# Optimization experiments

Measured on AMD Instinct MI355X. Metric: run time of the kernel, lower is better.

## Reference

```python
import jax, jax.numpy as jnp
import numpy as np
from jax.ops import segment_sum, segment_max

# Graph layout: B contiguous graphs of NPER nodes each
N, B, NPER, E, K = 32768, 32, 1024, 524288, 32
IN_DIM, HID = 64, 64
H1, H2 = 4, 2
NEG_ATTN, NEG_ACT = 0.2, 0.01  # DGL GATConv leaky slope; module's LeakyReLU slope


def _gat(x, src, dst, W, al, ar, H, D):
    # DGL GATConv, no bias, no residual, dropout=0
    f = (x @ W).reshape(N, H, D)                      # [N,H,D]
    el = jnp.einsum('nhd,hd->nh', f, al)              # src attention term
    er = jnp.einsum('nhd,hd->nh', f, ar)              # dst attention term
    e = jax.nn.leaky_relu(el[src] + er[dst], NEG_ATTN)  # [E,H]
    m = segment_max(e, dst, num_segments=N)
    m = jnp.where(jnp.isfinite(m), m, 0.0)            # guard isolated nodes
    p = jnp.exp(e - m[dst])
    z = segment_sum(p, dst, num_segments=N)
    a = p / jnp.maximum(z[dst], 1e-9)                 # edge softmax over in-edges
    return segment_sum(a[:, :, None] * f[src], dst, num_segments=N)  # [N,H,D]


def _graphnorm(x, alpha, gamma, beta, eps=1e-5):
    # GraphNorm (Cai et al.): per-graph node normalization with learnable mean scale
    xb = x.reshape(B, NPER, *x.shape[1:])
    mean = xb.mean(axis=1, keepdims=True)
    c = xb - alpha * mean
    var = (c * c).mean(axis=1, keepdims=True)
    return (gamma * c / jnp.sqrt(var + eps) + beta).reshape(x.shape)


def _sortpool(x):
    # DGL SortPooling: sort each node's features ascending, pick top-K nodes by last channel
    xs = jnp.sort(x, axis=-1).reshape(B, NPER, -1)
    _, idx = jax.lax.top_k(xs[:, :, -1], K)           # [B,K]
    sel = jnp.take_along_axis(xs, idx[:, :, None], axis=1)  # [B,K,D]
    return sel.reshape(B, -1)


def setup_inputs() -> dict:
    key = jax.random.key(0)
    ks = jax.random.split(key, 16)
    rng = np.random.default_rng(0)
    # edges constrained within each contiguous graph block
    g = rng.integers(0, B, size=E)
    src = (g * NPER + rng.integers(0, NPER, size=E)).astype(np.int32)
    dst = (g * NPER + rng.integers(0, NPER, size=E)).astype(np.int32)
    s = 0.05
    return {
        'features': jax.random.normal(ks[0], (N, IN_DIM), jnp.float32),
        'src': jnp.asarray(src), 'dst': jnp.asarray(dst),
        'W1': jax.random.normal(ks[1], (IN_DIM, H1 * HID), jnp.float32) * s,
        'al1': jax.random.normal(ks[2], (H1, HID), jnp.float32) * s,
        'ar1': jax.random.normal(ks[3], (H1, HID), jnp.float32) * s,
        'W2': jax.random.normal(ks[4], (H1 * HID, H2 * HID), jnp.float32) * s,
        'al2': jax.random.normal(ks[5], (H2, HID), jnp.float32) * s,
        'ar2': jax.random.normal(ks[6], (H2, HID), jnp.float32) * s,
        'gn1_alpha': jnp.ones((HID,), jnp.float32),
        'gn1_gamma': jnp.ones((HID,), jnp.float32),
        'gn1_beta': jnp.zeros((HID,), jnp.float32),
        'gn2_alpha': jnp.ones((HID,), jnp.float32),
        'gn2_gamma': jnp.ones((HID,), jnp.float32),
        'gn2_beta': jnp.zeros((HID,), jnp.float32),
        'fc1_w': jax.random.normal(ks[7], (2 * K * HID, K * HID), jnp.float32) * 0.02,
        'fc1_b': jnp.zeros((K * HID,), jnp.float32),
        'fc2_w': jax.random.normal(ks[8], (K * HID, 16), jnp.float32) * 0.02,
        'fc2_b': jnp.zeros((16,), jnp.float32),
    }


def reference(features, src, dst, W1, al1, ar1, W2, al2, ar2,
              gn1_alpha, gn1_gamma, gn1_beta, gn2_alpha, gn2_gamma, gn2_beta,
              fc1_w, fc1_b, fc2_w, fc2_b):
    h1 = _gat(features, src, dst, W1, al1, ar1, H1, HID)          # [N,4,HID]
    h1 = jax.nn.leaky_relu(_graphnorm(h1, gn1_alpha, gn1_gamma, gn1_beta), NEG_ACT)
    r1 = _sortpool(h1.mean(1))                                    # [B,K*HID]
    h2 = _gat(h1.reshape(N, -1), src, dst, W2, al2, ar2, H2, HID)  # [N,2,HID]
    h2 = jax.nn.leaky_relu(_graphnorm(h2, gn2_alpha, gn2_gamma, gn2_beta), NEG_ACT)
    r = jnp.concatenate([r1, _sortpool(h2.mean(1))], axis=1)      # [B,2*K*HID]
    hidden = jax.nn.relu(r @ fc1_w + fc1_b)
    return hidden @ fc2_w + fc2_b                                 # [B,16]
```

## Files before the change

kernel.cpp:

```cpp
#include <hip/hip_runtime.h>
#include <math.h>

#define NNODES 32768
#define NGRAPH 32
#define NPERG  1024
#define KSEL   32
#define FC1_KS 64

__device__ inline float wave_reduce_sum(float v) {
  #pragma unroll
  for (int off = 32; off > 0; off >>= 1) v += __shfl_xor(v, off, 64);
  return v;
}
__device__ inline float wave_reduce_max(float v) {
  #pragma unroll
  for (int off = 32; off > 0; off >>= 1) v = fmaxf(v, __shfl_xor(v, off, 64));
  return v;
}

__global__ void csr_count(const int* __restrict__ dst, int* __restrict__ counts, int E_) {
  int e = blockIdx.x * 256 + threadIdx.x;
  if (e < E_) atomicAdd(&counts[dst[e]], 1);
}

__global__ void csr_scan(const int* __restrict__ counts, int* __restrict__ rowptr,
                         int* __restrict__ cursor) {
  __shared__ int partial[256];
  int tid = threadIdx.x;
  int base = tid * 128;
  int s = 0;
  for (int i = 0; i < 128; ++i) s += counts[base + i];
  partial[tid] = s;
  __syncthreads();
  for (int off = 1; off < 256; off <<= 1) {
    int t = (tid >= off) ? partial[tid - off] : 0;
    __syncthreads();
    partial[tid] += t;
    __syncthreads();
  }
  int run = partial[tid] - s;
  for (int i = 0; i < 128; ++i) {
    int c = counts[base + i];
    rowptr[base + i] = run;
    cursor[base + i] = run;
    run += c;
  }
  if (tid == 255) rowptr[NNODES] = run;
}

__global__ void csr_fill(const int* __restrict__ src, const int* __restrict__ dst,
                         int* __restrict__ cursor, int* __restrict__ csrsrc, int E_) {
  int e = blockIdx.x * 256 + threadIdx.x;
  if (e < E_) {
    int p = atomicAdd(&cursor[dst[e]], 1);
    csrsrc[p] = src[e];
  }
}

template <int K, int C, int H>
__global__ __launch_bounds__(256) void gemm_fused(
    const float* __restrict__ X, const float* __restrict__ W,
    const float* __restrict__ al, const float* __restrict__ ar,
    float* __restrict__ F, float* __restrict__ el, float* __restrict__ er) {
  __shared__ float Xs[16][68];
  __shared__ float Ws[16][64];
  __shared__ float redl[64][16];
  __shared__ float redr[64][16];
  const int tid = threadIdx.x;
  const int tx = tid & 15, ty = tid >> 4;
  const int bx = blockIdx.x;
  const int xcd = bx & 7, pos = bx >> 3;
  const int gph = xcd + (pos >> 4) * 8;
  const int row0 = (gph * 16 + (pos & 15)) * 64;
  const int col0 = blockIdx.y * 64;

  float acc[4][4];
  #pragma unroll
  for (int i = 0; i < 4; ++i)
    #pragma unroll
    for (int j = 0; j < 4; ++j) acc[i][j] = 0.f;

  const int rld = tid >> 2;
  const int kq = (tid & 3) * 4;
  const int kw = tid >> 4;
  const int cw = (tid & 15) * 4;

  for (int kt = 0; kt < K; kt += 16) {
    float4 xv = *(const float4*)&X[(size_t)(row0 + rld) * K + kt + kq];
    Xs[kq + 0][rld] = xv.x; Xs[kq + 1][rld] = xv.y;
    Xs[kq + 2][rld] = xv.z; Xs[kq + 3][rld] = xv.w;
    *(float4*)&Ws[kw][cw] = *(const float4*)&W[(size_t)(kt + kw) * C + col0 + cw];
    __syncthreads();
    #pragma unroll
    for (int k = 0; k < 16; ++k) {
      float xr[4], wr[4];
      #pragma unroll
      for (int i = 0; i < 4; ++i) xr[i] = Xs[k][ty * 4 + i];
      #pragma unroll
      for (int j = 0; j < 4; ++j) wr[j] = Ws[k][tx * 4 + j];
      #pragma unroll
      for (int i = 0; i < 4; ++i)
        #pragma unroll
        for (int j = 0; j < 4; ++j) acc[i][j] = fmaf(xr[i], wr[j], acc[i][j]);
    }
    __syncthreads();
  }

  float av[4], rv[4];
  #pragma unroll
  for (int j = 0; j < 4; ++j) { av[j] = al[col0 + tx * 4 + j]; rv[j] = ar[col0 + tx * 4 + j]; }
  #pragma unroll
  for (int i = 0; i < 4; ++i) {
    float4 o = make_float4(acc[i][0], acc[i][1], acc[i][2], acc[i][3]);
    *(float4*)&F[(size_t)(row0 + ty * 4 + i) * C + col0 + tx * 4] = o;
    float pl = acc[i][0] * av[0] + acc[i][1] * av[1] + acc[i][2] * av[2] + acc[i][3] * av[3];
    float pr = acc[i][0] * rv[0] + acc[i][1] * rv[1] + acc[i][2] * rv[2] + acc[i][3] * rv[3];
    redl[ty * 4 + i][tx] = pl;
    redr[ty * 4 + i][tx] = pr;
  }
  __syncthreads();
  if (tid < 64) {
    float s = 0.f, t = 0.f;
    #pragma unroll
    for (int x = 0; x < 16; ++x) { s += redl[tid][x]; t += redr[tid][x]; }
    el[(row0 + tid) * H + blockIdx.y] = s;
    er[(row0 + tid) * H + blockIdx.y] = t;
  }
}

template <int H>
__device__ inline void load_ev(const float* __restrict__ el, int s, float* ev) {
  if constexpr (H == 4) {
    float4 t = *(const float4*)(el + (size_t)s * 4);
    ev[0] = t.x; ev[1] = t.y; ev[2] = t.z; ev[3] = t.w;
  } else {
    float2 t = *(const float2*)(el + (size_t)s * 2);
    ev[0] = t.x; ev[1] = t.y;
  }
}

template <int H>
__global__ __launch_bounds__(256) void gat_agg(
    const float* __restrict__ F, const float* __restrict__ el,
    const float* __restrict__ er, const int* __restrict__ rowptr,
    const int* __restrict__ csrsrc, float* __restrict__ out) {
  __shared__ float plds[4][64][H];
  __shared__ int slds[4][64];
  const int wave = threadIdx.x >> 6;
  const int lane = threadIdx.x & 63;
  const int wg = blockIdx.x;
  const int xcd = wg & 7, pos = wg >> 3;
  const int g = xcd + (pos >> 8) * 8;
  const int n = g * NPERG + (pos & 255) * 4 + wave;
  const int beg = rowptr[n], end = rowptr[n + 1];
  const int hsel = (H == 4) ? (lane >> 4) : (lane >> 5);

  float erh[H];
  #pragma unroll
  for (int h = 0; h < H; ++h) erh[h] = er[n * H + h];

  float accv[H], psum[H];
  #pragma unroll
  for (int h = 0; h < H; ++h) { accv[h] = 0.f; psum[h] = 0.f; }

  for (int cbeg = beg; cbeg < end; cbeg += 64) {
    int cnt = end - cbeg;
    if (cnt > 64) cnt = 64;
    float pv[H];
    int s = 0;
    #pragma unroll
    for (int h = 0; h < H; ++h) pv[h] = 0.f;
    if (lane < cnt) {
      s = csrsrc[cbeg + lane];
      float ev[H];
      load_ev<H>(el, s, ev);
      #pragma unroll
      for (int h = 0; h < H; ++h) {
        float e = ev[h] + erh[h];
        e = e >= 0.f ? e : 0.2f * e;
        pv[h] = __expf(e);
      }
    }
    #pragma unroll
    for (int h = 0; h < H; ++h) psum[h] += wave_reduce_sum(pv[h]);
    slds[wave][lane] = s;
    if constexpr (H == 4)
      *(float4*)&plds[wave][lane][0] = make_float4(pv[0], pv[1], pv[2], pv[3]);
    else
      *(float2*)&plds[wave][lane][0] = make_float2(pv[0], pv[1]);
    __builtin_amdgcn_s_waitcnt(0);

    int j = 0;
    for (; j + 4 <= cnt; j += 4) {
      int ss0 = slds[wave][j + 0], ss1 = slds[wave][j + 1];
      int ss2 = slds[wave][j + 2], ss3 = slds[wave][j + 3];
      float pb0 = plds[wave][j + 0][hsel], pb1 = plds[wave][j + 1][hsel];
      float pb2 = plds[wave][j + 2][hsel], pb3 = plds[wave][j + 3][hsel];
      if constexpr (H == 4) {
        float4 f0 = *(const float4*)&F[(size_t)ss0 * 256 + lane * 4];
        float4 f1 = *(const float4*)&F[(size_t)ss1 * 256 + lane * 4];
        float4 f2 = *(const float4*)&F[(size_t)ss2 * 256 + lane * 4];
        float4 f3 = *(const float4*)&F[(size_t)ss3 * 256 + lane * 4];
        accv[0] = fmaf(pb0, f0.x, accv[0]); accv[1] = fmaf(pb0, f0.y, accv[1]);
        accv[2] = fmaf(pb0, f0.z, accv[2]); accv[3] = fmaf(pb0, f0.w, accv[3]);
        accv[0] = fmaf(pb1, f1.x, accv[0]); accv[1] = fmaf(pb1, f1.y, accv[1]);
        accv[2] = fmaf(pb1, f1.z, accv[2]); accv[3] = fmaf(pb1, f1.w, accv[3]);
        accv[0] = fmaf(pb2, f2.x, accv[0]); accv[1] = fmaf(pb2, f2.y, accv[1]);
        accv[2] = fmaf(pb2, f2.z, accv[2]); accv[3] = fmaf(pb2, f2.w, accv[3]);
        accv[0] = fmaf(pb3, f3.x, accv[0]); accv[1] = fmaf(pb3, f3.y, accv[1]);
        accv[2] = fmaf(pb3, f3.z, accv[2]); accv[3] = fmaf(pb3, f3.w, accv[3]);
      } else {
        float2 f0 = *(const float2*)&F[(size_t)ss0 * 128 + lane * 2];
        float2 f1 = *(const float2*)&F[(size_t)ss1 * 128 + lane * 2];
        float2 f2 = *(const float2*)&F[(size_t)ss2 * 128 + lane * 2];
        float2 f3 = *(const float2*)&F[(size_t)ss3 * 128 + lane * 2];
        accv[0] = fmaf(pb0, f0.x, accv[0]); accv[1] = fmaf(pb0, f0.y, accv[1]);
        accv[0] = fmaf(pb1, f1.x, accv[0]); accv[1] = fmaf(pb1, f1.y, accv[1]);
        accv[0] = fmaf(pb2, f2.x, accv[0]); accv[1] = fmaf(pb2, f2.y, accv[1]);
        accv[0] = fmaf(pb3, f3.x, accv[0]); accv[1] = fmaf(pb3, f3.y, accv[1]);
      }
    }
    for (; j < cnt; ++j) {
      int ss = slds[wave][j];
      float pb = plds[wave][j][hsel];
      if constexpr (H == 4) {
        float4 fv = *(const float4*)&F[(size_t)ss * 256 + lane * 4];
        accv[0] = fmaf(pb, fv.x, accv[0]); accv[1] = fmaf(pb, fv.y, accv[1]);
        accv[2] = fmaf(pb, fv.z, accv[2]); accv[3] = fmaf(pb, fv.w, accv[3]);
      } else {
        float2 fv = *(const float2*)&F[(size_t)ss * 128 + lane * 2];
        accv[0] = fmaf(pb, fv.x, accv[0]); accv[1] = fmaf(pb, fv.y, accv[1]);
      }
    }
  }

  float z;
  if constexpr (H == 4)
    z = hsel == 0 ? psum[0] : hsel == 1 ? psum[1] : hsel == 2 ? psum[2] : psum[3];
  else
    z = hsel == 0 ? psum[0] : psum[1];
  float inv = 1.0f / fmaxf(z, 1e-9f);
  if constexpr (H == 4) {
    float4 o = make_float4(accv[0] * inv, accv[1] * inv, accv[2] * inv, accv[3] * inv);
    *(float4*)&out[(size_t)n * 256 + lane * 4] = o;
  } else {
    float2 o = make_float2(accv[0] * inv, accv[1] * inv);
    *(float2*)&out[(size_t)n * 128 + lane * 2] = o;
  }
}

template <int C>
__global__ void gn_stats_partial(const float* __restrict__ X, float* __restrict__ ps,
                                 float* __restrict__ ps2) {
  const int id = blockIdx.x;
  const int xcd = id & 7, pos = id >> 3;
  const int b = xcd + (pos >> 4) * 8;
  const int sgm = pos & 15;
  int ch = threadIdx.x;
  const float* p = X + ((size_t)b * NPERG + sgm * 64) * C + ch;
  float sx = 0.f, sx2 = 0.f;
  for (int i = 0; i < 64; ++i) { float x = p[(size_t)i * C]; sx += x; sx2 += x * x; }
  ps[(b * 16 + sgm) * C + ch] = sx;
  ps2[(b * 16 + sgm) * C + ch] = sx2;
}

template <int C>
__global__ void gn_stats_final(const float* __restrict__ ps, const float* __restrict__ ps2,
                               const float* __restrict__ alpha, const float* __restrict__ gamma,
                               const float* __restrict__ beta, float* __restrict__ scale,
                               float* __restrict__ shift) {
  int b = blockIdx.x, ch = threadIdx.x;
  float sx = 0.f, sx2 = 0.f;
  for (int s = 0; s < 16; ++s) { sx += ps[(b * 16 + s) * C + ch]; sx2 += ps2[(b * 16 + s) * C + ch]; }
  const float inv = 1.0f / (float)NPERG;
  float mu = sx * inv;
  int d = ch & 63;
  float a = alpha[d];
  float var = sx2 * inv - mu * mu * a * (2.f - a);
  float sc = gamma[d] / sqrtf(var + 1e-5f);
  scale[b * C + ch] = sc;
  shift[b * C + ch] = beta[d] - sc * a * mu;
}

__global__ void gn_apply1(const float* __restrict__ h1, const float* __restrict__ scale,
                          const float* __restrict__ shift, float* __restrict__ h1n,
                          float* __restrict__ keyb) {
  const int wg = blockIdx.x;
  const int xcd = wg & 7, pos = wg >> 3;
  const int g = xcd + (pos >> 8) * 8;
  const int n = g * NPERG + (pos & 255) * 4 + (threadIdx.x >> 6);
  const int d = threadIdx.x & 63;
  const int b = g;
  float s = 0.f;
  #pragma unroll
  for (int h = 0; h < 4; ++h) {
    int ch = h * 64 + d;
    float y = scale[b * 256 + ch] * h1[(size_t)n * 256 + ch] + shift[b * 256 + ch];
    y = y >= 0.f ? y : 0.01f * y;
    h1n[(size_t)n * 256 + ch] = y;
    s += y;
  }
  float key = wave_reduce_max(0.25f * s);
  if (d == 0) keyb[n] = key;
}

__global__ void gn_apply2(const float* __restrict__ h2, const float* __restrict__ scale,
                          const float* __restrict__ shift, float* __restrict__ keyb) {
  const int wg = blockIdx.x;
  const int xcd = wg & 7, pos = wg >> 3;
  const int g = xcd + (pos >> 8) * 8;
  const int n = g * NPERG + (pos & 255) * 4 + (threadIdx.x >> 6);
  const int d = threadIdx.x & 63;
  const int b = g;
  float s = 0.f;
  #pragma unroll
  for (int h = 0; h < 2; ++h) {
    int ch = h * 64 + d;
    float y = scale[b * 128 + ch] * h2[(size_t)n * 128 + ch] + shift[b * 128 + ch];
    y = y >= 0.f ? y : 0.01f * y;
    s += y;
  }
  float key = wave_reduce_max(0.5f * s);
  if (d == 0) keyb[n] = key;
}

__global__ __launch_bounds__(1024) void topk_sort(const float* __restrict__ keyb,
                                                  int* __restrict__ topk) {
  __shared__ unsigned long long lds[NPERG];
  const int b = blockIdx.x, tid = threadIdx.x;
  float f = keyb[b * NPERG + tid];
  unsigned int u = __float_as_uint(f);
  u = (u & 0x80000000u) ? ~u : (u | 0x80000000u);
  unsigned long long v = ((unsigned long long)u << 32) | (unsigned int)(NPERG - 1 - tid);
  for (int kk = 2; kk <= NPERG; kk <<= 1) {
    for (int j = kk >> 1; j > 0; j >>= 1) {
      unsigned long long o;
      if (j >= 64) {
        lds[tid] = v;
        __syncthreads();
        o = lds[tid ^ j];
        __syncthreads();
      } else {
        o = __shfl_xor(v, j, 64);
      }
      bool lower = (tid & j) == 0;
      bool desc = (tid & kk) == 0;
      unsigned long long mx = v > o ? v : o;
      unsigned long long mn = v > o ? o : v;
      v = (lower == desc) ? mx : mn;
    }
  }
  if (tid < KSEL) topk[b * KSEL + tid] = (int)(NPERG - 1 - (unsigned int)(v & 0xFFFFFFFFu));
}

__device__ inline float bitonic_sort64(float v, int lane) {
  #pragma unroll
  for (int kk = 2; kk <= 64; kk <<= 1) {
    #pragma unroll
    for (int j = kk >> 1; j > 0; j >>= 1) {
      float o = __shfl_xor(v, j, 64);
      bool lower = (lane & j) == 0;
      bool asc = (lane & kk) == 0;
      v = (lower == asc) ? fminf(v, o) : fmaxf(v, o);
    }
  }
  return v;
}

__global__ void sortsel1(const float* __restrict__ h1n, const int* __restrict__ topk,
                         float* __restrict__ r) {
  int wid = (blockIdx.x * blockDim.x + threadIdx.x) >> 6;
  int lane = threadIdx.x & 63;
  int b = wid >> 5, k = wid & 31;
  int node = b * NPERG + topk[b * KSEL + k];
  float s = 0.f;
  #pragma unroll
  for (int h = 0; h < 4; ++h) s += h1n[(size_t)node * 256 + h * 64 + lane];
  float v = bitonic_sort64(0.25f * s, lane);
  r[(size_t)b * 4096 + k * 64 + lane] = v;
}

__global__ void sortsel2(const float* __restrict__ h2, const float* __restrict__ scale,
                         const float* __restrict__ shift, const int* __restrict__ topk,
                         float* __restrict__ r) {
  int wid = (blockIdx.x * blockDim.x + threadIdx.x) >> 6;
  int lane = threadIdx.x & 63;
  int b = wid >> 5, k = wid & 31;
  int node = b * NPERG + topk[b * KSEL + k];
  float s = 0.f;
  #pragma unroll
  for (int h = 0; h < 2; ++h) {
    int ch = h * 64 + lane;
    float y = scale[b * 128 + ch] * h2[(size_t)node * 128 + ch] + shift[b * 128 + ch];
    y = y >= 0.f ? y : 0.01f * y;
    s += y;
  }
  float v = bitonic_sort64(0.5f * s, lane);
  r[(size_t)b * 4096 + 2048 + k * 64 + lane] = v;
}

__global__ __launch_bounds__(256) void fc1_partial(const float* __restrict__ r,
                                                   const float* __restrict__ w,
                                                   float* __restrict__ part) {
  __shared__ float rs_t[64][36];
  const int ks = blockIdx.x, nb = blockIdx.y;
  const int tid = threadIdx.x;
  const int tx = tid & 63;
  const int ty = tid >> 6;

  #pragma unroll
  for (int t = 0; t < 8; ++t) {
    int elem = t * 256 + tid;
    int m = elem >> 6, k = elem & 63;
    rs_t[k][m] = r[(size_t)m * 4096 + ks * 64 + k];
  }
  __syncthreads();

  const float* wp = w + (size_t)(ks * 64) * 2048 + nb * 256 + tx * 4;
  float4 acc[8];
  #pragma unroll
  for (int i = 0; i < 8; ++i) acc[i] = make_float4(0.f, 0.f, 0.f, 0.f);

  #pragma unroll 4
  for (int k = 0; k < 64; ++k) {
    float4 wv = *(const float4*)&wp[(size_t)k * 2048];
    float4 ra = *(const float4*)&rs_t[k][ty * 8];
    float4 rb = *(const float4*)&rs_t[k][ty * 8 + 4];
    float rr[8] = {ra.x, ra.y, ra.z, ra.w, rb.x, rb.y, rb.z, rb.w};
    #pragma unroll
    for (int i = 0; i < 8; ++i) {
      acc[i].x = fmaf(rr[i], wv.x, acc[i].x);
      acc[i].y = fmaf(rr[i], wv.y, acc[i].y);
      acc[i].z = fmaf(rr[i], wv.z, acc[i].z);
      acc[i].w = fmaf(rr[i], wv.w, acc[i].w);
    }
  }

  #pragma unroll
  for (int i = 0; i < 8; ++i) {
    int m = ty * 8 + i;
    *(float4*)&part[((size_t)ks * 32 + m) * 2048 + nb * 256 + tx * 4] = acc[i];
  }
}

__global__ __launch_bounds__(256) void fc1_reduce(const float* __restrict__ part,
                                                  const float* __restrict__ bias,
                                                  float* __restrict__ hidden) {
  int idx = blockIdx.x * 256 + threadIdx.x;
  int m = idx >> 9, n4 = idx & 511;
  const float* pp = part + (size_t)m * 2048 + n4 * 4;
  float4 b4 = *(const float4*)&bias[n4 * 4];
  float4 s = b4;
  #pragma unroll 8
  for (int ks = 0; ks < FC1_KS; ++ks) {
    float4 v = *(const float4*)&pp[(size_t)ks * 32 * 2048];
    s.x += v.x; s.y += v.y; s.z += v.z; s.w += v.w;
  }
  s.x = fmaxf(s.x, 0.f); s.y = fmaxf(s.y, 0.f);
  s.z = fmaxf(s.z, 0.f); s.w = fmaxf(s.w, 0.f);
  *(float4*)&hidden[(size_t)m * 2048 + n4 * 4] = s;
}

__global__ void fc2_kernel(const float* __restrict__ hidden, const float* __restrict__ w,
                           const float* __restrict__ bias, float* __restrict__ out) {
  int wid = (blockIdx.x * blockDim.x + threadIdx.x) >> 6;
  int lane = threadIdx.x & 63;
  int m = wid >> 4, o = wid & 15;
  float s = 0.f;
  for (int k = lane; k < 2048; k += 64) s = fmaf(hidden[(size_t)m * 2048 + k], w[k * 16 + o], s);
  s = wave_reduce_sum(s);
  if (lane == 0) out[m * 16 + o] = s + bias[o];
}

extern "C" void kernel_launch(void* const* d_in, const int* in_sizes, int n_in,
                              void* d_out, int out_size, void* d_ws, size_t ws_size,
                              hipStream_t stream) {
  const float* features = (const float*)d_in[0];
  const int* src = (const int*)d_in[1];
  const int* dst = (const int*)d_in[2];
  const float* W1 = (const float*)d_in[3];
  const float* al1 = (const float*)d_in[4];
  const float* ar1 = (const float*)d_in[5];
  const float* W2 = (const float*)d_in[6];
  const float* al2 = (const float*)d_in[7];
  const float* ar2 = (const float*)d_in[8];
  const float* gn1a = (const float*)d_in[9];
  const float* gn1g = (const float*)d_in[10];
  const float* gn1b = (const float*)d_in[11];
  const float* gn2a = (const float*)d_in[12];
  const float* gn2g = (const float*)d_in[13];
  const float* gn2b = (const float*)d_in[14];
  const float* fc1w = (const float*)d_in[15];
  const float* fc1b = (const float*)d_in[16];
  const float* fc2w = (const float*)d_in[17];
  const float* fc2b = (const float*)d_in[18];
  float* out = (float*)d_out;
  const int E_ = in_sizes[1];

  float* ws = (float*)d_ws;
  size_t off = 0;
  float* A = ws + off;      off += (size_t)NNODES * 256;
  float* Bb = ws + off;     off += (size_t)NNODES * 256;
  float* el1 = ws + off;    off += (size_t)NNODES * 4;
  float* er1 = ws + off;    off += (size_t)NNODES * 4;
  float* el2 = ws + off;    off += (size_t)NNODES * 2;
  float* er2 = ws + off;    off += (size_t)NNODES * 2;
  float* sc1 = ws + off;    off += 32 * 256;
  float* sh1 = ws + off;    off += 32 * 256;
  float* sc2 = ws + off;    off += 32 * 128;
  float* sh2 = ws + off;    off += 32 * 128;
  float* ps = ws + off;     off += 32 * 16 * 256;
  float* ps2 = ws + off;    off += 32 * 16 * 256;
  float* rbuf = ws + off;   off += 32 * 4096;
  float* keyb = ws + off;   off += NNODES;
  int* ibase = (int*)(ws + off);
  int* counts = ibase;
  int* rowptr = counts + NNODES;
  int* cursor = rowptr + NNODES + 1;
  int* csrsrc = cursor + NNODES;
  int* tk1 = csrsrc + E_;
  int* tk2 = tk1 + NGRAPH * KSEL;

  float* f1 = A;
  float* h1n = A;
  float* h1 = Bb;
  float* f2 = Bb;
  float* h2 = Bb + (size_t)NNODES * 128;
  float* part = A;
  float* hidden = A + (size_t)FC1_KS * 32 * 2048;

  hipMemsetAsync(counts, 0, NNODES * sizeof(int), stream);
  csr_count<<<(E_ + 255) / 256, 256, 0, stream>>>(dst, counts, E_);
  csr_scan<<<1, 256, 0, stream>>>(counts, rowptr, cursor);
  csr_fill<<<(E_ + 255) / 256, 256, 0, stream>>>(src, dst, cursor, csrsrc, E_);

  dim3 g1(NNODES / 64, 4);
  gemm_fused<64, 256, 4><<<g1, 256, 0, stream>>>(features, W1, al1, ar1, f1, el1, er1);
  gat_agg<4><<<NNODES / 4, 256, 0, stream>>>(f1, el1, er1, rowptr, csrsrc, h1);

  gn_stats_partial<256><<<NGRAPH * 16, 256, 0, stream>>>(h1, ps, ps2);
  gn_stats_final<256><<<NGRAPH, 256, 0, stream>>>(ps, ps2, gn1a, gn1g, gn1b, sc1, sh1);
  gn_apply1<<<NNODES / 4, 256, 0, stream>>>(h1, sc1, sh1, h1n, keyb);

  topk_sort<<<NGRAPH, 1024, 0, stream>>>(keyb, tk1);
  sortsel1<<<256, 256, 0, stream>>>(h1n, tk1, rbuf);

  dim3 g2(NNODES / 64, 2);
  gemm_fused<256, 128, 2><<<g2, 256, 0, stream>>>(h1n, W2, al2, ar2, f2, el2, er2);
  gat_agg<2><<<NNODES / 4, 256, 0, stream>>>(f2, el2, er2, rowptr, csrsrc, h2);

  gn_stats_partial<128><<<NGRAPH * 16, 128, 0, stream>>>(h2, ps, ps2);
  gn_stats_final<128><<<NGRAPH, 128, 0, stream>>>(ps, ps2, gn2a, gn2g, gn2b, sc2, sh2);
  gn_apply2<<<NNODES / 4, 256, 0, stream>>>(h2, sc2, sh2, keyb);

  topk_sort<<<NGRAPH, 1024, 0, stream>>>(keyb, tk2);
  sortsel2<<<256, 256, 0, stream>>>(h2, sc2, sh2, tk2, rbuf);

  dim3 gfc(FC1_KS, 8);
  fc1_partial<<<gfc, 256, 0, stream>>>(rbuf, fc1w, part);
  fc1_reduce<<<32 * 2048 / 1024, 256, 0, stream>>>(part, fc1b, hidden);
  fc2_kernel<<<128, 256, 0, stream>>>(hidden, fc2w, fc2b, out);
}
```

Baseline: 266.0 us.

## Fuse top-k sort with sort-pool selection and widen CSR scan

Merges the per-graph bitonic top-k kernel with the subsequent feature-gather and per-node sort into a single kernel per layer, so each block reads the sorted ranks from LDS instead of writing and rereading a top-k index buffer. This removes two kernel launches and a global round trip. Separately, the single-block CSR prefix scan now uses 1024 threads with 32 elements each, held in registers, instead of 256 threads with 128 each that read counts twice. The fused pool kernel runs only 32 blocks, so the gather phase gets less parallelism than the previous 256-block sortsel kernels.

```diff
diff --git a/kernel.cpp b/kernel.cpp
--- a/kernel.cpp
+++ b/kernel.cpp
@@ -23,29 +23,32 @@
   if (e < E_) atomicAdd(&counts[dst[e]], 1);
 }
 
-__global__ void csr_scan(const int* __restrict__ counts, int* __restrict__ rowptr,
-                         int* __restrict__ cursor) {
-  __shared__ int partial[256];
-  int tid = threadIdx.x;
-  int base = tid * 128;
+__global__ __launch_bounds__(1024) void csr_scan(const int* __restrict__ counts,
+                                                 int* __restrict__ rowptr,
+                                                 int* __restrict__ cursor) {
+  __shared__ int partial[1024];
+  const int tid = threadIdx.x;
+  const int base = tid * 32;
+  int c[32];
   int s = 0;
-  for (int i = 0; i < 128; ++i) s += counts[base + i];
+  #pragma unroll
+  for (int i = 0; i < 32; ++i) { c[i] = counts[base + i]; s += c[i]; }
   partial[tid] = s;
   __syncthreads();
-  for (int off = 1; off < 256; off <<= 1) {
+  for (int off = 1; off < 1024; off <<= 1) {
     int t = (tid >= off) ? partial[tid - off] : 0;
     __syncthreads();
     partial[tid] += t;
     __syncthreads();
   }
   int run = partial[tid] - s;
-  for (int i = 0; i < 128; ++i) {
-    int c = counts[base + i];
+  #pragma unroll
+  for (int i = 0; i < 32; ++i) {
     rowptr[base + i] = run;
     cursor[base + i] = run;
-    run += c;
-  }
-  if (tid == 255) rowptr[NNODES] = run;
+    run += c[i];
+  }
+  if (tid == 1023) rowptr[NNODES] = run;
 }
 
 __global__ void csr_fill(const int* __restrict__ src, const int* __restrict__ dst,
@@ -324,14 +327,22 @@
   if (d == 0) keyb[n] = key;
 }
 
-__global__ __launch_bounds__(1024) void topk_sort(const float* __restrict__ keyb,
-                                                  int* __restrict__ topk) {
-  __shared__ unsigned long long lds[NPERG];
-  const int b = blockIdx.x, tid = threadIdx.x;
-  float f = keyb[b * NPERG + tid];
-  unsigned int u = __float_as_uint(f);
-  u = (u & 0x80000000u) ? ~u : (u | 0x80000000u);
-  unsigned long long v = ((unsigned long long)u << 32) | (unsigned int)(NPERG - 1 - tid);
+__device__ inline float bitonic_sort64(float v, int lane) {
+  #pragma unroll
+  for (int kk = 2; kk <= 64; kk <<= 1) {
+    #pragma unroll
+    for (int j = kk >> 1; j > 0; j >>= 1) {
+      float o = __shfl_xor(v, j, 64);
+      bool lower = (lane & j) == 0;
+      bool asc = (lane & kk) == 0;
+      v = (lower == asc) ? fminf(v, o) : fmaxf(v, o);
+    }
+  }
+  return v;
+}
+
+__device__ inline void bitonic_sort1024(unsigned long long& v,
+                                        unsigned long long* lds, int tid) {
   for (int kk = 2; kk <= NPERG; kk <<= 1) {
     for (int j = kk >> 1; j > 0; j >>= 1) {
       unsigned long long o;
@@ -350,53 +361,63 @@
       v = (lower == desc) ? mx : mn;
     }
   }
-  if (tid < KSEL) topk[b * KSEL + tid] = (int)(NPERG - 1 - (unsigned int)(v & 0xFFFFFFFFu));
-}
-
-__device__ inline float bitonic_sort64(float v, int lane) {
-  #pragma unroll
-  for (int kk = 2; kk <= 64; kk <<= 1) {
-    #pragma unroll
-    for (int j = kk >> 1; j > 0; j >>= 1) {
-      float o = __shfl_xor(v, j, 64);
-      bool lower = (lane & j) == 0;
-      bool asc = (lane & kk) == 0;
-      v = (lower == asc) ? fminf(v, o) : fmaxf(v, o);
-    }
-  }
-  return v;
-}
-
-__global__ void sortsel1(const float* __restrict__ h1n, const int* __restrict__ topk,
-                         float* __restrict__ r) {
-  int wid = (blockIdx.x * blockDim.x + threadIdx.x) >> 6;
-  int lane = threadIdx.x & 63;
-  int b = wid >> 5, k = wid & 31;
-  int node = b * NPERG + topk[b * KSEL + k];
-  float s = 0.f;
-  #pragma unroll
-  for (int h = 0; h < 4; ++h) s += h1n[(size_t)node * 256 + h * 64 + lane];
-  float v = bitonic_sort64(0.25f * s, lane);
-  r[(size_t)b * 4096 + k * 64 + lane] = v;
-}
-
-__global__ void sortsel2(const float* __restrict__ h2, const float* __restrict__ scale,
-                         const float* __restrict__ shift, const int* __restrict__ topk,
-                         float* __restrict__ r) {
-  int wid = (blockIdx.x * blockDim.x + threadIdx.x) >> 6;
-  int lane = threadIdx.x & 63;
-  int b = wid >> 5, k = wid & 31;
-  int node = b * NPERG + topk[b * KSEL + k];
-  float s = 0.f;
-  #pragma unroll
-  for (int h = 0; h < 2; ++h) {
-    int ch = h * 64 + lane;
-    float y = scale[b * 128 + ch] * h2[(size_t)node * 128 + ch] + shift[b * 128 + ch];
-    y = y >= 0.f ? y : 0.01f * y;
-    s += y;
-  }
-  float v = bitonic_sort64(0.5f * s, lane);
-  r[(size_t)b * 4096 + 2048 + k * 64 + lane] = v;
+  lds[tid] = v;
+  __syncthreads();
+}
+
+__device__ inline unsigned long long pack_key(float f, int tid) {
+  unsigned int u = __float_as_uint(f);
+  u = (u & 0x80000000u) ? ~u : (u | 0x80000000u);
+  return ((unsigned long long)u << 32) | (unsigned int)(NPERG - 1 - tid);
+}
+
+__global__ __launch_bounds__(1024) void topk_pool1(const float* __restrict__ keyb,
+                                                   const float* __restrict__ h1n,
+                                                   float* __restrict__ r) {
+  __shared__ unsigned long long lds[NPERG];
+  const int b = blockIdx.x, tid = threadIdx.x;
+  unsigned long long v = pack_key(keyb[b * NPERG + tid], tid);
+  bitonic_sort1024(v, lds, tid);
+  const int wave = tid >> 6, lane = tid & 63;
+  #pragma unroll
+  for (int q = 0; q < 2; ++q) {
+    int rank = wave * 2 + q;
+    int node = (int)(NPERG - 1 - (unsigned int)(lds[rank] & 0xFFFFFFFFu));
+    size_t base = ((size_t)(b * NPERG + node)) * 256;
+    float s = 0.f;
+    #pragma unroll
+    for (int h = 0; h < 4; ++h) s += h1n[base + h * 64 + lane];
+    float val = bitonic_sort64(0.25f * s, lane);
+    r[(size_t)b * 4096 + rank * 64 + lane] = val;
+  }
+}
+
+__global__ __launch_bounds__(1024) void topk_pool2(const float* __restrict__ keyb,
+                                                   const float* __restrict__ h2,
+                                                   const float* __restrict__ scale,
+                                                   const float* __restrict__ shift,
+                                                   float* __restrict__ r) {
+  __shared__ unsigned long long lds[NPERG];
+  const int b = blockIdx.x, tid = threadIdx.x;
+  unsigned long long v = pack_key(keyb[b * NPERG + tid], tid);
+  bitonic_sort1024(v, lds, tid);
+  const int wave = tid >> 6, lane = tid & 63;
+  #pragma unroll
+  for (int q = 0; q < 2; ++q) {
+    int rank = wave * 2 + q;
+    int node = (int)(NPERG - 1 - (unsigned int)(lds[rank] & 0xFFFFFFFFu));
+    size_t base = ((size_t)(b * NPERG + node)) * 128;
+    float s = 0.f;
+    #pragma unroll
+    for (int h = 0; h < 2; ++h) {
+      int ch = h * 64 + lane;
+      float y = scale[b * 128 + ch] * h2[base + ch] + shift[b * 128 + ch];
+      y = y >= 0.f ? y : 0.01f * y;
+      s += y;
+    }
+    float val = bitonic_sort64(0.5f * s, lane);
+    r[(size_t)b * 4096 + 2048 + rank * 64 + lane] = val;
+  }
 }
 
 __global__ __launch_bounds__(256) void fc1_partial(const float* __restrict__ r,
@@ -518,8 +539,6 @@
   int* rowptr = counts + NNODES;
   int* cursor = rowptr + NNODES + 1;
   int* csrsrc = cursor + NNODES;
-  int* tk1 = csrsrc + E_;
-  int* tk2 = tk1 + NGRAPH * KSEL;
 
   float* f1 = A;
   float* h1n = A;
@@ -531,7 +550,7 @@
 
   hipMemsetAsync(counts, 0, NNODES * sizeof(int), stream);
   csr_count<<<(E_ + 255) / 256, 256, 0, stream>>>(dst, counts, E_);
-  csr_scan<<<1, 256, 0, stream>>>(counts, rowptr, cursor);
+  csr_scan<<<1, 1024, 0, stream>>>(counts, rowptr, cursor);
   csr_fill<<<(E_ + 255) / 256, 256, 0, stream>>>(src, dst, cursor, csrsrc, E_);
 
   dim3 g1(NNODES / 64, 4);
@@ -542,8 +561,7 @@
   gn_stats_final<256><<<NGRAPH, 256, 0, stream>>>(ps, ps2, gn1a, gn1g, gn1b, sc1, sh1);
   gn_apply1<<<NNODES / 4, 256, 0, stream>>>(h1, sc1, sh1, h1n, keyb);
 
-  topk_sort<<<NGRAPH, 1024, 0, stream>>>(keyb, tk1);
-  sortsel1<<<256, 256, 0, stream>>>(h1n, tk1, rbuf);
+  topk_pool1<<<NGRAPH, 1024, 0, stream>>>(keyb, h1n, rbuf);
 
   dim3 g2(NNODES / 64, 2);
   gemm_fused<256, 128, 2><<<g2, 256, 0, stream>>>(h1n, W2, al2, ar2, f2, el2, er2);
@@ -553,8 +571,7 @@
   gn_stats_final<128><<<NGRAPH, 128, 0, stream>>>(ps, ps2, gn2a, gn2g, gn2b, sc2, sh2);
   gn_apply2<<<NNODES / 4, 256, 0, stream>>>(h2, sc2, sh2, keyb);
 
-  topk_sort<<<NGRAPH, 1024, 0, stream>>>(keyb, tk2);
-  sortsel2<<<256, 256, 0, stream>>>(h2, sc2, sh2, tk2, rbuf);
+  topk_pool2<<<NGRAPH, 1024, 0, stream>>>(keyb, h2, sc2, sh2, rbuf);
 
   dim3 gfc(FC1_KS, 8);
   fc1_partial<<<gfc, 256, 0, stream>>>(rbuf, fc1w, part);
```

New measurement: 259.6 us. 2.4% less time.
